# Performance work log

Measured on AMD Instinct MI355X. Metric: run time of the kernel, lower is better.

The kernel has to match this reference:

```python
import jax, jax.numpy as jnp
import numpy as np

TRUNC = (24, 24, 24)
OUT = (32, 32, 32)


def setup_inputs() -> dict:
    key = jax.random.key(0)
    x = jax.random.normal(key, (8, 32, 48, 48, 48), dtype=jnp.float32)
    return {"x": x}


def reference(x):
    # "DCT" as implemented in the source: real part of an ortho-normalized 3D FFT
    x_dct = jnp.real(jnp.fft.fftn(x, axes=(2, 3, 4), norm='ortho'))
    # crop to low-frequency corner, zero-pad up to output_size
    x_crop = x_dct[:, :, :TRUNC[0], :TRUNC[1], :TRUNC[2]]
    pad = ((0, 0), (0, 0),
           (0, OUT[0] - TRUNC[0]),
           (0, OUT[1] - TRUNC[1]),
           (0, OUT[2] - TRUNC[2]))
    x_pad = jnp.pad(x_crop, pad)
    # inverse transform on the output_size grid, keep real part
    x_idct = jnp.real(jnp.fft.ifftn(x_pad, axes=(2, 3, 4), norm='ortho'))
    return x_idct
```

## Files before the change

kernel.cpp:

```cpp
#include <hip/hip_runtime.h>
#include <math.h>


#define TWO_PI_48 0.13089969389957470f
#define TWO_PI_32 0.19634954084936207f
#define NORM_F    1.6611664e-05f

typedef _Float16 half8  __attribute__((ext_vector_type(8)));
typedef _Float16 half4v __attribute__((ext_vector_type(4)));
typedef float    f32x4  __attribute__((ext_vector_type(4)));

__device__ _Float16 T1frag[2][3][2][64][8];
__device__ _Float16 T2frag[2][3][2][64][8];
__device__ __align__(16) _Float16 TK2frag[2][4][3][64][8];
__device__ __align__(16) _Float16 MB2frag[2][4][2][64][8];
__device__ __align__(16) _Float16 TB3frag[2][2][2][64][8];

__device__ int g_twdone = 0;

__global__ void k_init_tw() {
  if (g_twdone) return;
  const int idx = blockIdx.x * 256 + threadIdx.x;
  if (idx < 3072) {
    const int j  = idx & 7;
    const int l  = (idx >> 3) & 63;
    const int ks = (idx >> 9) & 1;
    const int t  = idx >> 10;
    const int k  = ks * 32 + (l >> 4) * 8 + j;
    {
      const int m = t * 16 + (l & 15);
      float v = 0.f;
      if (k < 48) {
        const float a = (float)(((m % 24) * k) % 48) * TWO_PI_48;
        v = (m < 24) ? cosf(a) : -sinf(a);
      }
      const _Float16 h = (_Float16)v;
      T1frag[0][t][ks][l][j] = h;
      T1frag[1][t][ks][l][j] = (_Float16)(v - (float)h);
    }
    {
      const int c = t * 16 + (l & 15);
      float v = 0.f;
      if (k < 48) {
        const float a = (float)(((c % 24) * k) % 48) * TWO_PI_48;
        v = (c < 24) ? cosf(a) : sinf(a);
      }
      const _Float16 h = (_Float16)v;
      T2frag[0][t][ks][l][j] = h;
      T2frag[1][t][ks][l][j] = (_Float16)(v - (float)h);
    }
  } else if (idx < 3072 + 6144) {
    const int local = idx - 3072;
    const int j = local & 7, l = (local >> 3) & 63;
    const int rest = local >> 9;
    const int ks = rest % 3, mt = rest / 3;
    const int m   = mt * 16 + (l & 15);
    const int kap = ks * 32 + (l >> 4) * 8 + j;
    const int n1  = kap % 48;
    const bool isVi = kap >= 48;
    const int m1  = m & 31;
    const bool isWi = m >= 32;
    float acc = 0.f;
    for (int k1 = 0; k1 < 24; ++k1) {
      float s32v, c32v, s48v, c48v;
      sincosf((float)((k1 * m1) % 32) * TWO_PI_32, &s32v, &c32v);
      sincosf((float)((k1 * n1) % 48) * TWO_PI_48, &s48v, &c48v);
      acc = fmaf(isWi ? s32v : c32v, isVi ? s48v : c48v, acc);
    }
    const _Float16 h = (_Float16)acc;
    TK2frag[0][mt][ks][l][j] = h;
    TK2frag[1][mt][ks][l][j] = (_Float16)(acc - (float)h);
  } else if (idx < 3072 + 6144 + 4096) {
    const int local = idx - (3072 + 6144);
    const int j = local & 7, l = (local >> 3) & 63;
    const int rest = local >> 9;
    const int ks = rest & 1, mt = rest >> 1;
    const int m   = mt * 16 + (l & 15);
    const int kap = ks * 32 + (l >> 4) * 8 + j;
    float v = 0.f;
    if (kap < 48) {
      const int k2 = kap % 24;
      const int m2 = m & 31;
      float s, c;
      sincosf((float)((k2 * m2) % 32) * TWO_PI_32, &s, &c);
      if (m < 32) v = (kap < 24) ? c : -s;
      else        v = (kap < 24) ? s :  c;
    }
    const _Float16 h = (_Float16)v;
    MB2frag[0][mt][ks][l][j] = h;
    MB2frag[1][mt][ks][l][j] = (_Float16)(v - (float)h);
  } else if (idx < 15360) {
    const int local = idx - (3072 + 6144 + 4096);
    const int j = local & 7, l = (local >> 3) & 63;
    const int rest = local >> 9;
    const int ks = rest & 1, nt = rest >> 1;
    const int m3  = nt * 16 + (l & 15);
    const int kap = ks * 32 + (l >> 4) * 8 + j;
    float v = 0.f;
    if (kap < 48) {
      const int k3 = kap % 24;
      float s, c;
      sincosf((float)((k3 * m3) % 32) * TWO_PI_32, &s, &c);
      v = (kap < 24) ? c : -s;
    }
    const _Float16 h = (_Float16)v;
    TB3frag[0][nt][ks][l][j] = h;
    TB3frag[1][nt][ks][l][j] = (_Float16)(v - (float)h);
  }
}

__device__ inline void split8(const float* qf, half8& h, half8& lo) {
#pragma unroll
  for (int j = 0; j < 8; ++j) {
    const _Float16 hh = (_Float16)qf[j];
    h[j]  = hh;
    lo[j] = (_Float16)(qf[j] - (float)hh);
  }
}

__global__ __launch_bounds__(64) void k1_waveslab(const float* __restrict__ x,
                                                  float2* __restrict__ V) {
  const int n1   = blockIdx.x;
  const int bc   = blockIdx.y;
  const int lane = threadIdx.x;

  __shared__ __align__(16) unsigned char arena[13824];
  _Float16* Uh = (_Float16*)arena;
  _Float16* Ul = (_Float16*)(arena + 6912);
  float*    D2 = (float*)arena;

  const int c16  = lane & 15;
  const int kgrp = lane >> 4;
  const int kb   = kgrp * 8;

  half8 t1h[3][2], t1l[3][2], t2h[3][2], t2l[3][2];
#pragma unroll
  for (int mt = 0; mt < 3; ++mt)
#pragma unroll
    for (int ks = 0; ks < 2; ++ks) {
      t1h[mt][ks] = *(const half8*)&T1frag[0][mt][ks][lane][0];
      t1l[mt][ks] = *(const half8*)&T1frag[1][mt][ks][lane][0];
      t2h[mt][ks] = *(const half8*)&T2frag[0][mt][ks][lane][0];
      t2l[mt][ks] = *(const half8*)&T2frag[1][mt][ks][lane][0];
    }

#pragma unroll
  for (int p = 0; p < 3; ++p) {
    const int i = lane + 64 * p;
    const int which = i / 48, r = i % 48;
    _Float16* base = (which & 2) ? Ul : Uh;
    *(half8*)&base[r * 72 + 48 + (which & 1) * 8] = (half8){};
  }

  const float* xs = x + (size_t)(bc * 48 + n1) * 2304;

  float4 fa0, fb0, fa1, fb1;
  {
    const float4* p0 = (const float4*)(xs + c16 * 48 + kb);
    fa0 = p0[0]; fb0 = p0[1];
    const int k1i = 32 + kb;
    if (k1i < 48) {
      const float4* p1 = (const float4*)(xs + c16 * 48 + k1i);
      fa1 = p1[0]; fb1 = p1[1];
    } else { fa1 = make_float4(0.f,0.f,0.f,0.f); fb1 = fa1; }
  }

#pragma unroll
  for (int nt = 0; nt < 3; ++nt) {
    float4 na0, nb0, na1, nb1;
    if (nt < 2) {
      const int c = (nt + 1) * 16 + c16;
      const float4* p0 = (const float4*)(xs + c * 48 + kb);
      na0 = p0[0]; nb0 = p0[1];
      const int k1i = 32 + kb;
      if (k1i < 48) {
        const float4* p1 = (const float4*)(xs + c * 48 + k1i);
        na1 = p1[0]; nb1 = p1[1];
      } else { na1 = make_float4(0.f,0.f,0.f,0.f); nb1 = na1; }
    }

    f32x4 acc0 = {}, acc1 = {}, acc2 = {};
#pragma unroll
    for (int ks = 0; ks < 2; ++ks) {
      const float4 qa = ks ? fa1 : fa0;
      const float4 qb = ks ? fb1 : fb0;
      const float qf[8] = {qa.x, qa.y, qa.z, qa.w, qb.x, qb.y, qb.z, qb.w};
      half8 bh, bl;
      split8(qf, bh, bl);
#pragma unroll
      for (int mt = 0; mt < 3; ++mt) {
        f32x4& acc = (mt == 0) ? acc0 : (mt == 1) ? acc1 : acc2;
        acc = __builtin_amdgcn_mfma_f32_16x16x32_f16(t1h[mt][ks], bh, acc, 0, 0, 0);
        acc = __builtin_amdgcn_mfma_f32_16x16x32_f16(t1h[mt][ks], bl, acc, 0, 0, 0);
        acc = __builtin_amdgcn_mfma_f32_16x16x32_f16(t1l[mt][ks], bh, acc, 0, 0, 0);
      }
    }

    {
      const int cc = nt * 16 + c16;
#pragma unroll
      for (int mt = 0; mt < 3; ++mt) {
        const int r0 = mt * 16 + kgrp * 4;
        const f32x4 acc = (mt == 0) ? acc0 : (mt == 1) ? acc1 : acc2;
#pragma unroll
        for (int r = 0; r < 4; ++r) {
          const float v = acc[r];
          const _Float16 h = (_Float16)v;
          Uh[(r0 + r) * 72 + cc] = h;
          Ul[(r0 + r) * 72 + cc] = (_Float16)(v - (float)h);
        }
      }
    }

    fa0 = na0; fb0 = nb0; fa1 = na1; fb1 = nb1;
  }

  f32x4 a2[3][3] = {};
#pragma unroll
  for (int ks = 0; ks < 2; ++ks) {
#pragma unroll
    for (int mt = 0; mt < 3; ++mt) {
      const half8 ah = *(const half8*)&Uh[(mt * 16 + c16) * 72 + ks * 32 + kb];
      const half8 al = *(const half8*)&Ul[(mt * 16 + c16) * 72 + ks * 32 + kb];
#pragma unroll
      for (int nt2 = 0; nt2 < 3; ++nt2) {
        a2[mt][nt2] = __builtin_amdgcn_mfma_f32_16x16x32_f16(ah, t2h[nt2][ks], a2[mt][nt2], 0, 0, 0);
        a2[mt][nt2] = __builtin_amdgcn_mfma_f32_16x16x32_f16(ah, t2l[nt2][ks], a2[mt][nt2], 0, 0, 0);
        a2[mt][nt2] = __builtin_amdgcn_mfma_f32_16x16x32_f16(al, t2h[nt2][ks], a2[mt][nt2], 0, 0, 0);
      }
    }
  }

#pragma unroll
  for (int mt = 0; mt < 3; ++mt)
#pragma unroll
    for (int nt2 = 0; nt2 < 3; ++nt2) {
      const int r0 = mt * 16 + kgrp * 4;
      const int cc = nt2 * 16 + c16;
#pragma unroll
      for (int r = 0; r < 4; ++r)
        D2[(r0 + r) * 68 + cc] = a2[mt][nt2][r];
    }

#pragma unroll
  for (int q = 0; q < 9; ++q) {
    const int idx = lane + 64 * q;
    const int k3 = idx / 24, k2 = idx % 24;
    const float grr = D2[k3 * 68 + k2];
    const float gis = D2[(k3 + 24) * 68 + k2 + 24];
    const float gir = D2[(k3 + 24) * 68 + k2];
    const float grs = D2[k3 * 68 + k2 + 24];
    V[(size_t)bc * 27648 + (size_t)k3 * 1152 + n1 * 24 + k2] =
        make_float2(grr + gis, gir - grs);
  }
}

__global__ __launch_bounds__(192) void k2_mfma(const float2* __restrict__ V,
                                               float2* __restrict__ W) {
  const int k3   = blockIdx.x;
  const int byy  = blockIdx.y;
  const int tid  = threadIdx.x;
  const int lane = tid & 63;
  const int w    = tid >> 6;

  __shared__ __align__(16) float Bb[48 * 100];

  half8 kth[4][3], ktl[4][3];
#pragma unroll
  for (int mt = 0; mt < 4; ++mt)
#pragma unroll
    for (int ks = 0; ks < 3; ++ks) {
      kth[mt][ks] = *(const half8*)&TK2frag[0][mt][ks][lane][0];
      ktl[mt][ks] = *(const half8*)&TK2frag[1][mt][ks][lane][0];
    }

  const int kbase = (lane >> 4) * 8;
  const int c16   = lane & 15;
  const int cc    = w * 16 + c16;
  const int sE    = cc / 24, k2E = cc % 24;
  const int rbase = (lane >> 4) * 4;

  float4 vr[6];
  {
    const float4* g0 = (const float4*)(V + ((size_t)((byy * 4 + 0) * 24 + k3)) * 1152);
    const float4* g1 = (const float4*)(V + ((size_t)((byy * 4 + 1) * 24 + k3)) * 1152);
#pragma unroll
    for (int jj = 0; jj < 6; ++jj)
      vr[jj] = (jj < 3 ? g0 : g1)[tid + 192 * (jj % 3)];
  }

  for (int g = 0; g < 2; ++g) {
    const int bcp = byy * 2 + g;

    if (g) __syncthreads();

#pragma unroll
    for (int jj = 0; jj < 6; ++jj) {
      const int s = jj / 3;
      const int r = tid + 192 * (jj % 3);
      const int n1 = r / 12, c4 = r % 12;
      const float4 f = vr[jj];
      float* bp = &Bb[(s * 24 + c4 * 2) * 100 + n1];
      bp[0]   = f.x;  bp[48]  = f.y;
      bp[100] = f.z;  bp[148] = f.w;
    }
    if (g < 1) {
      const float4* g0 = (const float4*)(V + ((size_t)((bcp * 2 + 2) * 24 + k3)) * 1152);
      const float4* g1 = (const float4*)(V + ((size_t)((bcp * 2 + 3) * 24 + k3)) * 1152);
#pragma unroll
      for (int jj = 0; jj < 6; ++jj)
        vr[jj] = (jj < 3 ? g0 : g1)[tid + 192 * (jj % 3)];
    }
    __syncthreads();

    f32x4 a0 = {}, a1 = {}, a2 = {}, a3 = {};
#pragma unroll
    for (int ks = 0; ks < 3; ++ks) {
      const float4 q0 = *(const float4*)&Bb[cc * 100 + ks * 32 + kbase];
      const float4 q1 = *(const float4*)&Bb[cc * 100 + ks * 32 + kbase + 4];
      const float qf[8] = {q0.x, q0.y, q0.z, q0.w, q1.x, q1.y, q1.z, q1.w};
      half8 bh, bl;
      split8(qf, bh, bl);
#pragma unroll
      for (int mt = 0; mt < 4; ++mt) {
        f32x4& acc = (mt == 0) ? a0 : (mt == 1) ? a1 : (mt == 2) ? a2 : a3;
        acc = __builtin_amdgcn_mfma_f32_16x16x32_f16(kth[mt][ks], bh, acc, 0, 0, 0);
        acc = __builtin_amdgcn_mfma_f32_16x16x32_f16(kth[mt][ks], bl, acc, 0, 0, 0);
        acc = __builtin_amdgcn_mfma_f32_16x16x32_f16(ktl[mt][ks], bh, acc, 0, 0, 0);
      }
    }

    const int bc = bcp * 2 + sE;
    float2* wp = W + (size_t)bc * 18432 + (size_t)k3 * 24 + k2E;
#pragma unroll
    for (int mt = 0; mt < 2; ++mt) {
      const f32x4 wr = (mt == 0) ? a0 : a1;
      const f32x4 wi = (mt == 0) ? a2 : a3;
#pragma unroll
      for (int r = 0; r < 4; ++r) {
        const int m1 = mt * 16 + rbase + r;
        wp[(size_t)m1 * 576] = make_float2(wr[r], wi[r]);
      }
    }
  }
}

__global__ __launch_bounds__(128) void k3_mfma(const float2* __restrict__ W,
                                               float* __restrict__ out) {
  const int m1   = blockIdx.x;
  const int byy  = blockIdx.y;
  const int tid  = threadIdx.x;
  const int lane = tid & 63;
  const int w    = tid >> 6;

  __shared__ __align__(16) float Bt[32 * 68];
  __shared__ __align__(16) float Zb[32 * 68];

  half8 mbh[4][2], mbl[4][2];
#pragma unroll
  for (int mt = 0; mt < 4; ++mt)
#pragma unroll
    for (int ks = 0; ks < 2; ++ks) {
      mbh[mt][ks] = *(const half8*)&MB2frag[0][mt][ks][lane][0];
      mbl[mt][ks] = *(const half8*)&MB2frag[1][mt][ks][lane][0];
    }
  half8 tb3h[2], tb3l[2];
#pragma unroll
  for (int ks = 0; ks < 2; ++ks) {
    tb3h[ks] = *(const half8*)&TB3frag[0][w][ks][lane][0];
    tb3l[ks] = *(const half8*)&TB3frag[1][w][ks][lane][0];
  }

  for (int i = tid; i < 8 * 68; i += 128)  Bt[(24 + i / 68) * 68 + (i % 68)] = 0.f;
  for (int i = tid; i < 24 * 20; i += 128) Bt[(i / 20) * 68 + 48 + (i % 20)] = 0.f;
  for (int i = tid; i < 32 * 20; i += 128) Zb[(i / 20) * 68 + 48 + (i % 20)] = 0.f;

  const int kbase = (lane >> 4) * 8;
  const int c16   = lane & 15;
  const int cc    = w * 16 + c16;
  const int rbase = (lane >> 4) * 4;

  float4 vr0, vr1, vr2;
  {
    const float4* g4 = (const float4*)(W + (size_t)(byy * 2) * 18432 + (size_t)m1 * 576);
    vr0 = g4[tid];
    vr1 = g4[tid + 128];
    if (tid < 32) vr2 = g4[tid + 256];
  }

  for (int g = 0; g < 2; ++g) {
    const int bc = byy * 2 + g;

    {
      const float4 fr[3] = {vr0, vr1, vr2};
#pragma unroll
      for (int jj = 0; jj < 3; ++jj) {
        const int i4 = tid + 128 * jj;
        if (jj < 2 || tid < 32) {
          const int k3 = i4 / 12, c4 = i4 % 12;
          const float4 f = fr[jj];
          Bt[k3 * 68 + 2 * c4]          = f.x;
          Bt[k3 * 68 + 24 + 2 * c4]     = f.y;
          Bt[k3 * 68 + 2 * c4 + 1]      = f.z;
          Bt[k3 * 68 + 24 + 2 * c4 + 1] = f.w;
        }
      }
    }
    if (g < 1) {
      const float4* g4 = (const float4*)(W + (size_t)(bc + 1) * 18432 + (size_t)m1 * 576);
      vr0 = g4[tid];
      vr1 = g4[tid + 128];
      if (tid < 32) vr2 = g4[tid + 256];
    }
    __syncthreads();

    f32x4 z0 = {}, z1 = {}, z2 = {}, z3 = {};
#pragma unroll
    for (int ks = 0; ks < 2; ++ks) {
      const float4 q0 = *(const float4*)&Bt[cc * 68 + ks * 32 + kbase];
      const float4 q1 = *(const float4*)&Bt[cc * 68 + ks * 32 + kbase + 4];
      const float qf[8] = {q0.x, q0.y, q0.z, q0.w, q1.x, q1.y, q1.z, q1.w};
      half8 bh, bl;
      split8(qf, bh, bl);
#pragma unroll
      for (int mt = 0; mt < 4; ++mt) {
        f32x4& acc = (mt == 0) ? z0 : (mt == 1) ? z1 : (mt == 2) ? z2 : z3;
        acc = __builtin_amdgcn_mfma_f32_16x16x32_f16(mbh[mt][ks], bh, acc, 0, 0, 0);
        acc = __builtin_amdgcn_mfma_f32_16x16x32_f16(mbh[mt][ks], bl, acc, 0, 0, 0);
        acc = __builtin_amdgcn_mfma_f32_16x16x32_f16(mbl[mt][ks], bh, acc, 0, 0, 0);
      }
    }
    if (cc < 24) {
#pragma unroll
      for (int mt = 0; mt < 4; ++mt) {
        const f32x4 acc = (mt == 0) ? z0 : (mt == 1) ? z1 : (mt == 2) ? z2 : z3;
        const int row0 = mt * 16 + rbase;
#pragma unroll
        for (int r = 0; r < 4; ++r) {
          const int row = row0 + r;
          if (row < 32) Zb[row * 68 + cc]              = acc[r];
          else          Zb[(row - 32) * 68 + 24 + cc]  = acc[r];
        }
      }
    }
    __syncthreads();

    f32x4 o0 = {}, o1 = {};
#pragma unroll
    for (int ks = 0; ks < 2; ++ks) {
#pragma unroll
      for (int mt = 0; mt < 2; ++mt) {
        const float4 q0 = *(const float4*)&Zb[(mt * 16 + c16) * 68 + ks * 32 + kbase];
        const float4 q1 = *(const float4*)&Zb[(mt * 16 + c16) * 68 + ks * 32 + kbase + 4];
        const float qf[8] = {q0.x, q0.y, q0.z, q0.w, q1.x, q1.y, q1.z, q1.w};
        half8 ah, al;
        split8(qf, ah, al);
        f32x4& acc = (mt == 0) ? o0 : o1;
        acc = __builtin_amdgcn_mfma_f32_16x16x32_f16(ah, tb3h[ks], acc, 0, 0, 0);
        acc = __builtin_amdgcn_mfma_f32_16x16x32_f16(ah, tb3l[ks], acc, 0, 0, 0);
        acc = __builtin_amdgcn_mfma_f32_16x16x32_f16(al, tb3h[ks], acc, 0, 0, 0);
      }
    }
    float* op = out + (size_t)(bc * 32 + m1) * 1024;
#pragma unroll
    for (int mt = 0; mt < 2; ++mt) {
      const f32x4 acc = (mt == 0) ? o0 : o1;
#pragma unroll
      for (int r = 0; r < 4; ++r) {
        const int m2 = mt * 16 + rbase + r;
        op[m2 * 32 + cc] = acc[r] * NORM_F;
      }
    }
  }

  if (tid == 0 && blockIdx.x == 0 && blockIdx.y == 0) g_twdone = 1;
}

extern "C" void kernel_launch(void* const* d_in, const int* in_sizes, int n_in,
                              void* d_out, int out_size, void* d_ws, size_t ws_size,
                              hipStream_t stream) {
  const float* x = (const float*)d_in[0];
  float* out = (float*)d_out;
  float2* V = (float2*)d_ws;
  float2* W = (float2*)((char*)d_ws + 56623104);

  k_init_tw   <<<dim3(60), dim3(256), 0, stream>>>();
  k1_waveslab <<<dim3(48, 256), dim3(64), 0, stream>>>(x, V);
  k2_mfma     <<<dim3(24, 64), dim3(192), 0, stream>>>(V, W);
  k3_mfma     <<<dim3(32, 128), dim3(128), 0, stream>>>(W, out);
}
```

Baseline: 80.11 us.

## Split pipeline into four batch chunks across concurrent streams

```diff
diff --git a/kernel.cpp b/kernel.cpp
--- a/kernel.cpp
+++ b/kernel.cpp
@@ -119,9 +119,10 @@
 }
 
 __global__ __launch_bounds__(64) void k1_waveslab(const float* __restrict__ x,
-                                                  float2* __restrict__ V) {
+                                                  float2* __restrict__ V,
+                                                  const int bc0) {
   const int n1   = blockIdx.x;
-  const int bc   = blockIdx.y;
+  const int bc   = blockIdx.y + bc0;
   const int lane = threadIdx.x;
 
   __shared__ __align__(16) unsigned char arena[13824];
@@ -132,17 +133,6 @@
   const int c16  = lane & 15;
   const int kgrp = lane >> 4;
   const int kb   = kgrp * 8;
-
-  half8 t1h[3][2], t1l[3][2], t2h[3][2], t2l[3][2];
-#pragma unroll
-  for (int mt = 0; mt < 3; ++mt)
-#pragma unroll
-    for (int ks = 0; ks < 2; ++ks) {
-      t1h[mt][ks] = *(const half8*)&T1frag[0][mt][ks][lane][0];
-      t1l[mt][ks] = *(const half8*)&T1frag[1][mt][ks][lane][0];
-      t2h[mt][ks] = *(const half8*)&T2frag[0][mt][ks][lane][0];
-      t2l[mt][ks] = *(const half8*)&T2frag[1][mt][ks][lane][0];
-    }
 
 #pragma unroll
   for (int p = 0; p < 3; ++p) {
@@ -189,10 +179,12 @@
       split8(qf, bh, bl);
 #pragma unroll
       for (int mt = 0; mt < 3; ++mt) {
+        const half8 th = *(const half8*)&T1frag[0][mt][ks][lane][0];
+        const half8 tl = *(const half8*)&T1frag[1][mt][ks][lane][0];
         f32x4& acc = (mt == 0) ? acc0 : (mt == 1) ? acc1 : acc2;
-        acc = __builtin_amdgcn_mfma_f32_16x16x32_f16(t1h[mt][ks], bh, acc, 0, 0, 0);
-        acc = __builtin_amdgcn_mfma_f32_16x16x32_f16(t1h[mt][ks], bl, acc, 0, 0, 0);
-        acc = __builtin_amdgcn_mfma_f32_16x16x32_f16(t1l[mt][ks], bh, acc, 0, 0, 0);
+        acc = __builtin_amdgcn_mfma_f32_16x16x32_f16(th, bh, acc, 0, 0, 0);
+        acc = __builtin_amdgcn_mfma_f32_16x16x32_f16(th, bl, acc, 0, 0, 0);
+        acc = __builtin_amdgcn_mfma_f32_16x16x32_f16(tl, bh, acc, 0, 0, 0);
       }
     }
 
@@ -218,15 +210,21 @@
   f32x4 a2[3][3] = {};
 #pragma unroll
   for (int ks = 0; ks < 2; ++ks) {
+    half8 t2hk[3], t2lk[3];
+#pragma unroll
+    for (int nt2 = 0; nt2 < 3; ++nt2) {
+      t2hk[nt2] = *(const half8*)&T2frag[0][nt2][ks][lane][0];
+      t2lk[nt2] = *(const half8*)&T2frag[1][nt2][ks][lane][0];
+    }
 #pragma unroll
     for (int mt = 0; mt < 3; ++mt) {
       const half8 ah = *(const half8*)&Uh[(mt * 16 + c16) * 72 + ks * 32 + kb];
       const half8 al = *(const half8*)&Ul[(mt * 16 + c16) * 72 + ks * 32 + kb];
 #pragma unroll
       for (int nt2 = 0; nt2 < 3; ++nt2) {
-        a2[mt][nt2] = __builtin_amdgcn_mfma_f32_16x16x32_f16(ah, t2h[nt2][ks], a2[mt][nt2], 0, 0, 0);
-        a2[mt][nt2] = __builtin_amdgcn_mfma_f32_16x16x32_f16(ah, t2l[nt2][ks], a2[mt][nt2], 0, 0, 0);
-        a2[mt][nt2] = __builtin_amdgcn_mfma_f32_16x16x32_f16(al, t2h[nt2][ks], a2[mt][nt2], 0, 0, 0);
+        a2[mt][nt2] = __builtin_amdgcn_mfma_f32_16x16x32_f16(ah, t2hk[nt2], a2[mt][nt2], 0, 0, 0);
+        a2[mt][nt2] = __builtin_amdgcn_mfma_f32_16x16x32_f16(ah, t2lk[nt2], a2[mt][nt2], 0, 0, 0);
+        a2[mt][nt2] = __builtin_amdgcn_mfma_f32_16x16x32_f16(al, t2hk[nt2], a2[mt][nt2], 0, 0, 0);
       }
     }
   }
@@ -256,9 +254,10 @@
 }
 
 __global__ __launch_bounds__(192) void k2_mfma(const float2* __restrict__ V,
-                                               float2* __restrict__ W) {
+                                               float2* __restrict__ W,
+                                               const int byy0) {
   const int k3   = blockIdx.x;
-  const int byy  = blockIdx.y;
+  const int byy  = blockIdx.y + byy0;
   const int tid  = threadIdx.x;
   const int lane = tid & 63;
   const int w    = tid >> 6;
@@ -346,9 +345,10 @@
 }
 
 __global__ __launch_bounds__(128) void k3_mfma(const float2* __restrict__ W,
-                                               float* __restrict__ out) {
+                                               float* __restrict__ out,
+                                               const int byy0) {
   const int m1   = blockIdx.x;
-  const int byy  = blockIdx.y;
+  const int byy  = blockIdx.y + byy0;
   const int tid  = threadIdx.x;
   const int lane = tid & 63;
   const int w    = tid >> 6;
@@ -484,8 +484,29 @@
   float2* V = (float2*)d_ws;
   float2* W = (float2*)((char*)d_ws + 56623104);
 
-  k_init_tw   <<<dim3(60), dim3(256), 0, stream>>>();
-  k1_waveslab <<<dim3(48, 256), dim3(64), 0, stream>>>(x, V);
-  k2_mfma     <<<dim3(24, 64), dim3(192), 0, stream>>>(V, W);
-  k3_mfma     <<<dim3(32, 128), dim3(128), 0, stream>>>(W, out);
+  static hipStream_t side[3];
+  static hipEvent_t  evInit, evDone[3];
+  static bool once = false;
+  if (!once) {
+    for (int i = 0; i < 3; ++i) hipStreamCreateWithFlags(&side[i], hipStreamNonBlocking);
+    hipEventCreateWithFlags(&evInit, hipEventDisableTiming);
+    for (int i = 0; i < 3; ++i) hipEventCreateWithFlags(&evDone[i], hipEventDisableTiming);
+    once = true;
+  }
+
+  k_init_tw<<<dim3(60), dim3(256), 0, stream>>>();
+  hipEventRecord(evInit, stream);
+  for (int i = 0; i < 3; ++i) hipStreamWaitEvent(side[i], evInit, 0);
+
+  for (int c = 0; c < 4; ++c) {
+    hipStream_t sc = (c == 0) ? stream : side[c - 1];
+    k1_waveslab<<<dim3(48, 64), dim3(64),  0, sc>>>(x, V, c * 64);
+    k2_mfma    <<<dim3(24, 16), dim3(192), 0, sc>>>(V, W, c * 16);
+    k3_mfma    <<<dim3(32, 32), dim3(128), 0, sc>>>(W, out, c * 32);
+  }
+
+  for (int i = 0; i < 3; ++i) {
+    hipEventRecord(evDone[i], side[i]);
+    hipStreamWaitEvent(stream, evDone[i], 0);
+  }
 }
```

Result: slower. 122.3 us (+52.7%).
